# Kernel tuning notes

Hardware: AMD Instinct MI355X
Metric: run time of the kernel (lower is better)

## Reference

```python
import jax, jax.numpy as jnp
import numpy as np

N = 50000
E = 800000
IN_DIM = 128
HEADS = 4
OUT_DIM = 32
TOT = HEADS * OUT_DIM  # 128 == IN_DIM -> residual_proj is None
LN_EPS = 1e-5
NEG_SLOPE = 0.2


def setup_inputs() -> dict:
    key = jax.random.key(0)
    ks = jax.random.split(key, 10)
    x = jax.random.normal(ks[0], (N, IN_DIM), dtype=jnp.float32)
    # random edges guaranteed src != dst (PyG GATv2Conv removes then re-adds self loops)
    src = jax.random.randint(ks[1], (E,), 0, N)
    off = jax.random.randint(ks[2], (E,), 1, N)
    dst = (src + off) % N
    edge_index = jnp.stack([src, dst]).astype(jnp.int64)
    # glorot-style init for weights
    sc = 1.0 / np.sqrt(IN_DIM)
    W_l = jax.random.uniform(ks[3], (IN_DIM, TOT), jnp.float32, -sc, sc)
    b_l = jnp.zeros((TOT,), jnp.float32)
    W_r = jax.random.uniform(ks[4], (IN_DIM, TOT), jnp.float32, -sc, sc)
    b_r = jnp.zeros((TOT,), jnp.float32)
    att = jax.random.uniform(ks[5], (HEADS, OUT_DIM), jnp.float32, -sc, sc)
    bias = jnp.zeros((TOT,), jnp.float32)
    ln_g = jnp.ones((TOT,), jnp.float32)
    ln_b = jnp.zeros((TOT,), jnp.float32)
    return {"x": x, "edge_index": edge_index, "W_l": W_l, "b_l": b_l,
            "W_r": W_r, "b_r": b_r, "att": att, "bias": bias,
            "ln_g": ln_g, "ln_b": ln_b}


def _gatv2_layer(x, src, dst, W_l, b_l, W_r, b_r, att, bias, ln_g, ln_b):
    n = x.shape[0]
    # GATv2Conv: x_l = lin_l(x) (source/messages), x_r = lin_r(x) (target)
    xl = (x @ W_l + b_l).reshape(n, HEADS, OUT_DIM)
    xr = (x @ W_r + b_r).reshape(n, HEADS, OUT_DIM)
    m = xl[src] + xr[dst]                               # [E+N, H, D]
    s = jnp.einsum('ehd,hd->eh', jax.nn.leaky_relu(m, NEG_SLOPE), att)
    # per-destination softmax (every node has a self loop -> no empty segments)
    smax = jax.ops.segment_max(s, dst, num_segments=n)  # [N, H]
    e = jnp.exp(s - smax[dst])
    denom = jax.ops.segment_sum(e, dst, num_segments=n)
    alpha = e / denom[dst]                              # [E+N, H]
    out = jax.ops.segment_sum(alpha[..., None] * xl[src], dst, num_segments=n)
    out = out.reshape(n, TOT) + bias
    out = out + x                                       # residual (in_dim == total_out_dim)
    mu = jnp.mean(out, axis=-1, keepdims=True)
    var = jnp.mean(jnp.square(out - mu), axis=-1, keepdims=True)
    y = (out - mu) / jnp.sqrt(var + LN_EPS) * ln_g + ln_b
    return jax.nn.elu(y)


def reference(x, edge_index, W_l, b_l, W_r, b_r, att, bias, ln_g, ln_b):
    n = x.shape[0]
    loops = jnp.arange(n, dtype=edge_index.dtype)
    src = jnp.concatenate([edge_index[0], loops])
    dst = jnp.concatenate([edge_index[1], loops])
    return _gatv2_layer(x, src, dst, W_l, b_l, W_r, b_r, att, bias, ln_g, ln_b)
```

## Files before the change

### kernel.cpp

```cpp
#include <hip/hip_runtime.h>

#define N_NODES 50000
#define E_EDGES 800000
#define M_TOTAL (E_EDGES + N_NODES)
#define IN_DIM 128
#define HEADS 4
#define OUT_DIM 32
#define TOT 128
#define LN_EPS 1e-5f
#define NEG_SLOPE 0.2f
#define LOG2E 1.4426950408889634f

#define SCAN_NBLK ((N_NODES + 255) / 256)
#define GEMM_NBLK ((N_NODES + 63) / 64)
#define HIST_NBLK 64
#define EPB 13312
#define SEPB (EPB / 8)
#define SCAT_NBLK (HIST_NBLK * 8)

typedef __bf16 bf16x8 __attribute__((ext_vector_type(8)));
typedef float  f32x4  __attribute__((ext_vector_type(4)));
typedef _Float16 h2   __attribute__((ext_vector_type(2)));

__device__ __forceinline__ float quad_sum(float p) {
    p += __int_as_float(__builtin_amdgcn_update_dpp(
        0, __float_as_int(p), 0xB1 , 0xF, 0xF, true));
    p += __int_as_float(__builtin_amdgcn_update_dpp(
        0, __float_as_int(p), 0x4E , 0xF, 0xF, true));
    return p;
}

__global__ __launch_bounds__(256) void wthist_kernel(
    const int* __restrict__ dsts,
    const float* __restrict__ Wl, const float* __restrict__ Wr,
    unsigned* __restrict__ WT, unsigned char* __restrict__ HP,
    unsigned char* __restrict__ rank8) {
    __shared__ unsigned cnt[N_NODES / 8];
    const int b = blockIdx.x, t = threadIdx.x;
    if (b < 64) {
        const int u = b * 256 + t;
        const int col = u >> 6, k2 = u & 63;
        const float* __restrict__ W = (col < 128) ? Wl : Wr;
        const int c = col & 127;
        union { __bf16 bb[2]; unsigned uu; } p;
        p.bb[0] = (__bf16)W[(2 * k2) * TOT + c];
        p.bb[1] = (__bf16)W[(2 * k2 + 1) * TOT + c];
        WT[col * 64 + k2] = p.uu;
        return;
    }
    const int hb = b - 64;
    const int m_begin = hb * EPB;
    const int m_end = min(m_begin + EPB, M_TOTAL);
    for (int i = t; i < N_NODES / 8; i += 256) cnt[i] = 0;
    __syncthreads();
    for (int m0 = m_begin + t * 4; m0 < m_end; m0 += 1024) {
        int d[4];
        if (m0 < E_EDGES) {
            const int4 dv = *(const int4*)&dsts[m0];
            d[0] = dv.x; d[1] = dv.y; d[2] = dv.z; d[3] = dv.w;
        } else {
            d[0] = m0 - E_EDGES; d[1] = d[0] + 1; d[2] = d[0] + 2; d[3] = d[0] + 3;
        }
        uchar4 r;
        unsigned old, sh;
        sh = (d[0] & 7) * 4; old = atomicAdd(&cnt[d[0] >> 3], 1u << sh);
        r.x = (unsigned char)((old >> sh) & 15u);
        sh = (d[1] & 7) * 4; old = atomicAdd(&cnt[d[1] >> 3], 1u << sh);
        r.y = (unsigned char)((old >> sh) & 15u);
        sh = (d[2] & 7) * 4; old = atomicAdd(&cnt[d[2] >> 3], 1u << sh);
        r.z = (unsigned char)((old >> sh) & 15u);
        sh = (d[3] & 7) * 4; old = atomicAdd(&cnt[d[3] >> 3], 1u << sh);
        r.w = (unsigned char)((old >> sh) & 15u);
        *(uchar4*)&rank8[m0] = r;
    }
    __syncthreads();
    unsigned* __restrict__ Hrow = (unsigned*)(HP + (size_t)hb * N_NODES);
    for (int i = t; i < N_NODES / 8; i += 256) {
        const unsigned w = cnt[i];
        const unsigned lo = (w & 15u) | (((w >> 4) & 15u) << 8) |
                            (((w >> 8) & 15u) << 16) | (((w >> 12) & 15u) << 24);
        const unsigned hi = ((w >> 16) & 15u) | (((w >> 20) & 15u) << 8) |
                            (((w >> 24) & 15u) << 16) | (((w >> 28) & 15u) << 24);
        *(uint2*)&Hrow[2 * i] = make_uint2(lo, hi);
    }
}

__global__ __launch_bounds__(256) void scan1_kernel(
    unsigned char* __restrict__ HP,
    int* __restrict__ rowptr, int* __restrict__ blockSums) {
    __shared__ int sh[256];
    const int t = threadIdx.x;
    const int i = blockIdx.x * 256 + t;
    int tot = 0;
    if (i < N_NODES) {
        int run = 0;
#pragma unroll 16
        for (int b = 0; b < HIST_NBLK; ++b) {
            const int h = HP[(size_t)b * N_NODES + i];
            HP[(size_t)b * N_NODES + i] = (unsigned char)run;
            run += h;
        }
        tot = run;
    }
    sh[t] = tot;
    __syncthreads();
#pragma unroll
    for (int off = 1; off < 256; off <<= 1) {
        int u = (t >= off) ? sh[t - off] : 0;
        __syncthreads();
        sh[t] += u;
        __syncthreads();
    }
    if (i < N_NODES) rowptr[i] = sh[t] - tot;
    if (t == 255) blockSums[blockIdx.x] = sh[255];
}

__global__ __launch_bounds__(256) void scan23_kernel(
    const int* __restrict__ blockSums,
    int* __restrict__ rowptr ,
    unsigned short* __restrict__ sorted16) {
    __shared__ int sh[256];
    const int t = threadIdx.x;
    const int v0 = (t < SCAN_NBLK) ? blockSums[t] : 0;
    sh[t] = v0;
    __syncthreads();
#pragma unroll
    for (int off = 1; off < 256; off <<= 1) {
        int u = (t >= off) ? sh[t - off] : 0;
        __syncthreads();
        sh[t] += u;
        __syncthreads();
    }
    const int blockOff = (blockIdx.x == 0) ? 0 : sh[blockIdx.x - 1];
    const int i = blockIdx.x * 256 + t;
    if (i < N_NODES) rowptr[i] += blockOff;
    if (i == 0) rowptr[N_NODES] = M_TOTAL;
    if (blockIdx.x == 0 && t < 32) sorted16[M_TOTAL + t] = 0;
}

__global__ __launch_bounds__(256) void gemmscatter_kernel(
    const float* __restrict__ x, const unsigned* __restrict__ WT,
    const float* __restrict__ bl, const float* __restrict__ br,
    unsigned* __restrict__ xlb, unsigned* __restrict__ xrb,
    const int* __restrict__ srcs, const int* __restrict__ dsts,
    const int* __restrict__ rowptr, const unsigned char* __restrict__ P,
    const unsigned char* __restrict__ rank8,
    unsigned short* __restrict__ sorted16) {
    __shared__ float epi[4][16][66];
    __shared__ unsigned Bs[64][68];
    const int t = threadIdx.x;
    if (blockIdx.x >= GEMM_NBLK) {
        const int sb = blockIdx.x - GEMM_NBLK;
        const int hb = sb >> 3;
        const unsigned char* __restrict__ Pb = P + (size_t)hb * N_NODES;
        const int eb = hb * EPB + (sb & 7) * SEPB;
        const int ee = min(eb + SEPB, M_TOTAL);
        for (int m0 = eb + t * 4; m0 < ee; m0 += 1024) {
            int s[4], d[4];
            if (m0 < E_EDGES) {
                const int4 sv = *(const int4*)&srcs[m0];
                const int4 dv = *(const int4*)&dsts[m0];
                s[0] = sv.x; s[1] = sv.y; s[2] = sv.z; s[3] = sv.w;
                d[0] = dv.x; d[1] = dv.y; d[2] = dv.z; d[3] = dv.w;
            } else {
                s[0] = d[0] = m0 - E_EDGES;
                s[1] = d[1] = d[0] + 1; s[2] = d[2] = d[0] + 2; s[3] = d[3] = d[0] + 3;
            }
            const uchar4 r = *(const uchar4*)&rank8[m0];
            sorted16[rowptr[d[0]] + (int)Pb[d[0]] + (int)r.x] = (unsigned short)s[0];
            sorted16[rowptr[d[1]] + (int)Pb[d[1]] + (int)r.y] = (unsigned short)s[1];
            sorted16[rowptr[d[2]] + (int)Pb[d[2]] + (int)r.z] = (unsigned short)s[2];
            sorted16[rowptr[d[3]] + (int)Pb[d[3]] + (int)r.w] = (unsigned short)s[3];
        }
        return;
    }
    const int w = t >> 6, lane = t & 63;
    const int q = lane >> 4, ln = lane & 15;
    const int m0 = blockIdx.x * 64;

    const int row = min(m0 + w * 16 + ln, N_NODES - 1);
    const float* __restrict__ xrow = x + (size_t)row * IN_DIM;
    bf16x8 A[4];
#pragma unroll
    for (int c = 0; c < 4; ++c) {
        const float4 v0 = *(const float4*)&xrow[c * 32 + q * 8];
        const float4 v1 = *(const float4*)&xrow[c * 32 + q * 8 + 4];
        bf16x8 a;
        a[0] = (__bf16)v0.x; a[1] = (__bf16)v0.y; a[2] = (__bf16)v0.z; a[3] = (__bf16)v0.w;
        a[4] = (__bf16)v1.x; a[5] = (__bf16)v1.y; a[6] = (__bf16)v1.z; a[7] = (__bf16)v1.w;
        A[c] = a;
    }

    const int mr = lane >> 2, cg2 = (lane & 3) * 16;
    const int grow = m0 + w * 16 + mr;
#pragma unroll
    for (int g = 0; g < 4; ++g) {
        const int n0 = g * 64;
        __syncthreads();
        {
            const unsigned* __restrict__ src = WT + n0 * 64;
#pragma unroll
            for (int it = 0; it < 4; ++it) {
                const int dw = t * 4 + it * 1024;
                const uint4 v = *(const uint4*)&src[dw];
                *(uint4*)&Bs[dw >> 6][dw & 63] = v;
            }
        }
        __syncthreads();
        const float* __restrict__ bvec = (g < 2) ? bl : br;
        f32x4 acc[4];
#pragma unroll
        for (int nt = 0; nt < 4; ++nt) {
            const float b = bvec[(n0 & 127) + nt * 16 + ln];
            acc[nt] = (f32x4){b, b, b, b};
        }
#pragma unroll
        for (int nt = 0; nt < 4; ++nt) {
#pragma unroll
            for (int c = 0; c < 4; ++c) {
                const bf16x8 B = *(const bf16x8*)&Bs[nt * 16 + ln][c * 16 + q * 4];
                acc[nt] = __builtin_amdgcn_mfma_f32_16x16x32_bf16(A[c], B, acc[nt], 0, 0, 0);
            }
        }
#pragma unroll
        for (int nt = 0; nt < 4; ++nt)
#pragma unroll
            for (int r = 0; r < 4; ++r)
                epi[w][q * 4 + r][nt * 16 + ln] = acc[nt][r];

        if (grow < N_NODES) {
            unsigned p[8];
#pragma unroll
            for (int i = 0; i < 8; ++i) {
                union { _Float16 h[2]; unsigned u; } pk;
                pk.h[0] = (_Float16)epi[w][mr][cg2 + 2 * i];
                pk.h[1] = (_Float16)epi[w][mr][cg2 + 2 * i + 1];
                p[i] = pk.u;
            }
            unsigned* __restrict__ dst = ((g < 2) ? xlb : xrb) +
                (size_t)grow * 64 + (g & 1) * 32 + (cg2 >> 1);
            *(uint4*)&dst[0] = make_uint4(p[0], p[1], p[2], p[3]);
            *(uint4*)&dst[4] = make_uint4(p[4], p[5], p[6], p[7]);
        }
    }
}

__global__ __launch_bounds__(256) void gat_kernel(
    const int* __restrict__ rowptr, const unsigned short* __restrict__ sorted16,
    const unsigned* __restrict__ xlb, const unsigned* __restrict__ xrb,
    const float* __restrict__ att, const float* __restrict__ x,
    const float* __restrict__ bias, const float* __restrict__ g,
    const float* __restrict__ bvec, float* __restrict__ out) {
    const int d = blockIdx.x * 4 + (threadIdx.x >> 6);
    const int lane = threadIdx.x & 63;
    const int ln = lane & 15, q = lane >> 4;
    if (d >= N_NODES) return;

    h2 xrh[4], ath[4];
    {
        const uint4 ur = *(const uint4*)&xrb[(size_t)d * 64 + 4 * ln];
        union { uint4 u; h2 h[4]; } cr; cr.u = ur;
        xrh[0] = cr.h[0]; xrh[1] = cr.h[1]; xrh[2] = cr.h[2]; xrh[3] = cr.h[3];
        const float4 a0 = *(const float4*)&att[8 * ln];
        const float4 a1 = *(const float4*)&att[8 * ln + 4];
        ath[0][0] = (_Float16)(a0.x * LOG2E); ath[0][1] = (_Float16)(a0.y * LOG2E);
        ath[1][0] = (_Float16)(a0.z * LOG2E); ath[1][1] = (_Float16)(a0.w * LOG2E);
        ath[2][0] = (_Float16)(a1.x * LOG2E); ath[2][1] = (_Float16)(a1.y * LOG2E);
        ath[3][0] = (_Float16)(a1.z * LOG2E); ath[3][1] = (_Float16)(a1.w * LOG2E);
    }
    const h2 slope = (h2){(_Float16)NEG_SLOPE, (_Float16)NEG_SLOPE};
    const int beg = rowptr[d], end = rowptr[d + 1];

    float l = 0.f;
    h2 acc4[4];
#pragma unroll
    for (int k = 0; k < 4; ++k) acc4[k] = (h2){(_Float16)0.f, (_Float16)0.f};

    uint4 u0, u1;
    {
        const int sA0 = (int)sorted16[min(beg + q, end - 1)];
        const int sA1 = (int)sorted16[min(beg + 4 + q, end - 1)];
        u0 = *(const uint4*)&xlb[(size_t)sA0 * 64 + 4 * ln];
        u1 = *(const uint4*)&xlb[(size_t)sA1 * 64 + 4 * ln];
    }
    int sB0 = (int)sorted16[min(beg + 8 + q, end - 1)];
    int sB1 = (int)sorted16[min(beg + 12 + q, end - 1)];

    for (int base = beg; base < end; base += 8) {
        const int sC0 = (int)sorted16[min(base + 16 + q, end - 1)];
        const int sC1 = (int)sorted16[min(base + 20 + q, end - 1)];
        const uint4 un0 = *(const uint4*)&xlb[(size_t)sB0 * 64 + 4 * ln];
        const uint4 un1 = *(const uint4*)&xlb[(size_t)sB1 * 64 + 4 * ln];

        union { unsigned uu; h2 h; } a0, a1, a2, a3, b0, b1, b2, b3;
        a0.uu = u0.x; a1.uu = u0.y; a2.uu = u0.z; a3.uu = u0.w;
        b0.uu = u1.x; b1.uu = u1.y; b2.uu = u1.z; b3.uu = u1.w;
        h2 mA0 = a0.h + xrh[0], mA1 = a1.h + xrh[1];
        h2 mA2 = a2.h + xrh[2], mA3 = a3.h + xrh[3];
        h2 mB0 = b0.h + xrh[0], mB1 = b1.h + xrh[1];
        h2 mB2 = b2.h + xrh[2], mB3 = b3.h + xrh[3];
        mA0 = __builtin_elementwise_max(mA0, mA0 * slope);
        mA1 = __builtin_elementwise_max(mA1, mA1 * slope);
        mA2 = __builtin_elementwise_max(mA2, mA2 * slope);
        mA3 = __builtin_elementwise_max(mA3, mA3 * slope);
        mB0 = __builtin_elementwise_max(mB0, mB0 * slope);
        mB1 = __builtin_elementwise_max(mB1, mB1 * slope);
        mB2 = __builtin_elementwise_max(mB2, mB2 * slope);
        mB3 = __builtin_elementwise_max(mB3, mB3 * slope);
        float p0 = __builtin_amdgcn_fdot2(mA0, ath[0], 0.0f, false);
        p0 = __builtin_amdgcn_fdot2(mA1, ath[1], p0, false);
        p0 = __builtin_amdgcn_fdot2(mA2, ath[2], p0, false);
        p0 = __builtin_amdgcn_fdot2(mA3, ath[3], p0, false);
        float p1 = __builtin_amdgcn_fdot2(mB0, ath[0], 0.0f, false);
        p1 = __builtin_amdgcn_fdot2(mB1, ath[1], p1, false);
        p1 = __builtin_amdgcn_fdot2(mB2, ath[2], p1, false);
        p1 = __builtin_amdgcn_fdot2(mB3, ath[3], p1, false);
        p0 = quad_sum(p0);
        p1 = quad_sum(p1);
        const float e0 = (base + q < end) ? exp2f(p0) : 0.f;
        const float e1 = (base + 4 + q < end) ? exp2f(p1) : 0.f;
        l += e0 + e1;
        const _Float16 eh0 = (_Float16)e0, eh1 = (_Float16)e1;
        const h2 e20 = (h2){eh0, eh0}, e21 = (h2){eh1, eh1};
        acc4[0] += e20 * a0.h; acc4[0] += e21 * b0.h;
        acc4[1] += e20 * a1.h; acc4[1] += e21 * b1.h;
        acc4[2] += e20 * a2.h; acc4[2] += e21 * b2.h;
        acc4[3] += e20 * a3.h; acc4[3] += e21 * b3.h;

        u0 = un0; u1 = un1; sB0 = sC0; sB1 = sC1;
    }

#pragma unroll
    for (int off = 16; off <= 32; off <<= 1) {
        l += __shfl_xor(l, off, 64);
#pragma unroll
        for (int k = 0; k < 4; ++k) {
            union { h2 h; int i; } tmp; tmp.h = acc4[k];
            tmp.i = __shfl_xor(tmp.i, off, 64);
            acc4[k] += tmp.h;
        }
    }
    float acc[8];
#pragma unroll
    for (int k = 0; k < 4; ++k) {
        acc[2 * k]     = (float)acc4[k][0];
        acc[2 * k + 1] = (float)acc4[k][1];
    }

    const float inv_l = 1.0f / l;
    const float4 xv0 = *(const float4*)&x[(size_t)d * TOT + 8 * ln];
    const float4 xv1 = *(const float4*)&x[(size_t)d * TOT + 8 * ln + 4];
    const float4 bi0 = *(const float4*)&bias[8 * ln];
    const float4 bi1 = *(const float4*)&bias[8 * ln + 4];
    float v[8];
    v[0] = fmaf(acc[0], inv_l, bi0.x + xv0.x);
    v[1] = fmaf(acc[1], inv_l, bi0.y + xv0.y);
    v[2] = fmaf(acc[2], inv_l, bi0.z + xv0.z);
    v[3] = fmaf(acc[3], inv_l, bi0.w + xv0.w);
    v[4] = fmaf(acc[4], inv_l, bi1.x + xv1.x);
    v[5] = fmaf(acc[5], inv_l, bi1.y + xv1.y);
    v[6] = fmaf(acc[6], inv_l, bi1.z + xv1.z);
    v[7] = fmaf(acc[7], inv_l, bi1.w + xv1.w);
    float sum = 0.f, sq = 0.f;
#pragma unroll
    for (int k = 0; k < 8; ++k) { sum += v[k]; sq = fmaf(v[k], v[k], sq); }
#pragma unroll
    for (int off = 1; off <= 8; off <<= 1) {
        sum += __shfl_xor(sum, off, 64);
        sq  += __shfl_xor(sq,  off, 64);
    }
    const float mu  = sum * (1.0f / TOT);
    const float var = sq * (1.0f / TOT) - mu * mu;
    const float inv = rsqrtf(var + LN_EPS);
    const float4 g0 = *(const float4*)&g[8 * ln];
    const float4 g1 = *(const float4*)&g[8 * ln + 4];
    const float4 b0 = *(const float4*)&bvec[8 * ln];
    const float4 b1 = *(const float4*)&bvec[8 * ln + 4];
    float y[8];
    y[0] = (v[0] - mu) * inv * g0.x + b0.x;
    y[1] = (v[1] - mu) * inv * g0.y + b0.y;
    y[2] = (v[2] - mu) * inv * g0.z + b0.z;
    y[3] = (v[3] - mu) * inv * g0.w + b0.w;
    y[4] = (v[4] - mu) * inv * g1.x + b1.x;
    y[5] = (v[5] - mu) * inv * g1.y + b1.y;
    y[6] = (v[6] - mu) * inv * g1.z + b1.z;
    y[7] = (v[7] - mu) * inv * g1.w + b1.w;
#pragma unroll
    for (int k = 0; k < 8; ++k) y[k] = y[k] > 0.f ? y[k] : __expf(y[k]) - 1.f;
    if (q < 2) {
        float4 o = (q == 0) ? make_float4(y[0], y[1], y[2], y[3])
                            : make_float4(y[4], y[5], y[6], y[7]);
        *(float4*)&out[(size_t)d * TOT + 8 * ln + 4 * q] = o;
    }
}

extern "C" void kernel_launch(void* const* d_in, const int* in_sizes, int n_in,
                              void* d_out, int out_size, void* d_ws, size_t ws_size,
                              hipStream_t stream) {
    const float* x    = (const float*)d_in[0];
    const int*   ei   = (const int*)d_in[1];
    const float* Wl   = (const float*)d_in[2];
    const float* bl   = (const float*)d_in[3];
    const float* Wr   = (const float*)d_in[4];
    const float* br   = (const float*)d_in[5];
    const float* att  = (const float*)d_in[6];
    const float* bias = (const float*)d_in[7];
    const float* ln_g = (const float*)d_in[8];
    const float* ln_b = (const float*)d_in[9];
    const int* srcs = ei;
    const int* dsts = ei + E_EDGES;

    unsigned* xlb = (unsigned*)d_ws;
    unsigned* xrb = xlb + (size_t)N_NODES * 64;
    int*   rowptr     = (int*)(xrb + (size_t)N_NODES * 64);
    int*   blockSums  = rowptr + N_NODES + 1;
    unsigned* WT      = (unsigned*)(blockSums + SCAN_NBLK + 4);
    unsigned char* HP = (unsigned char*)(WT + 256 * 64);
    unsigned short* sorted16 = (unsigned short*)(HP + (size_t)HIST_NBLK * N_NODES);
    unsigned char*  rank8    = (unsigned char*)(sorted16 + M_TOTAL + 32);

    wthist_kernel<<<64 + HIST_NBLK, 256, 0, stream>>>(dsts, Wl, Wr, WT, HP, rank8);
    scan1_kernel<<<SCAN_NBLK, 256, 0, stream>>>(HP, rowptr, blockSums);
    scan23_kernel<<<SCAN_NBLK, 256, 0, stream>>>(blockSums, rowptr, sorted16);
    gemmscatter_kernel<<<GEMM_NBLK + SCAT_NBLK, 256, 0, stream>>>(
        x, WT, bl, br, xlb, xrb, srcs, dsts, rowptr, HP, rank8, sorted16);
    gat_kernel<<<(N_NODES + 3) / 4, 256, 0, stream>>>(rowptr, sorted16, xlb, xrb, att, x,
                                                      bias, ln_g, ln_b, (float*)d_out);
}
```

Baseline: 172.0 us.

## Fuse two-pass scan into single-pass lookback scan and deepen gather prefetch

```diff
diff --git a/kernel.cpp b/kernel.cpp
--- a/kernel.cpp
+++ b/kernel.cpp
@@ -34,10 +34,11 @@
     const int* __restrict__ dsts,
     const float* __restrict__ Wl, const float* __restrict__ Wr,
     unsigned* __restrict__ WT, unsigned char* __restrict__ HP,
-    unsigned char* __restrict__ rank8) {
+    unsigned char* __restrict__ rank8, unsigned* __restrict__ pub) {
     __shared__ unsigned cnt[N_NODES / 8];
     const int b = blockIdx.x, t = threadIdx.x;
     if (b < 64) {
+        if (b == 0 && t < SCAN_NBLK) pub[t] = 0;
         const int u = b * 256 + t;
         const int col = u >> 6, k2 = u & 63;
         const float* __restrict__ W = (col < 128) ? Wl : Wr;
@@ -85,12 +86,12 @@
     }
 }
 
-__global__ __launch_bounds__(256) void scan1_kernel(
-    unsigned char* __restrict__ HP,
-    int* __restrict__ rowptr, int* __restrict__ blockSums) {
+__global__ __launch_bounds__(256) void scan_kernel(
+    unsigned char* __restrict__ HP, int* __restrict__ rowptr,
+    unsigned* __restrict__ pub, unsigned short* __restrict__ sorted16) {
     __shared__ int sh[256];
-    const int t = threadIdx.x;
-    const int i = blockIdx.x * 256 + t;
+    const int t = threadIdx.x, bid = blockIdx.x;
+    const int i = bid * 256 + t;
     int tot = 0;
     if (i < N_NODES) {
         int run = 0;
@@ -111,31 +112,26 @@
         sh[t] += u;
         __syncthreads();
     }
-    if (i < N_NODES) rowptr[i] = sh[t] - tot;
-    if (t == 255) blockSums[blockIdx.x] = sh[255];
-}
-
-__global__ __launch_bounds__(256) void scan23_kernel(
-    const int* __restrict__ blockSums,
-    int* __restrict__ rowptr ,
-    unsigned short* __restrict__ sorted16) {
-    __shared__ int sh[256];
-    const int t = threadIdx.x;
-    const int v0 = (t < SCAN_NBLK) ? blockSums[t] : 0;
-    sh[t] = v0;
+    const int excl = sh[t] - tot;
+    if (t == 255) atomicExch(&pub[bid], (unsigned)(sh[255] + 1));
+    int part = 0;
+    for (int j = t; j < bid; j += 256) {
+        unsigned v;
+        do { v = atomicAdd(&pub[j], 0u); } while (v == 0u);
+        part += (int)v - 1;
+    }
     __syncthreads();
-#pragma unroll
-    for (int off = 1; off < 256; off <<= 1) {
-        int u = (t >= off) ? sh[t - off] : 0;
+    sh[t] = part;
+    __syncthreads();
+#pragma unroll
+    for (int off = 128; off >= 1; off >>= 1) {
+        if (t < off) sh[t] += sh[t + off];
         __syncthreads();
-        sh[t] += u;
-        __syncthreads();
-    }
-    const int blockOff = (blockIdx.x == 0) ? 0 : sh[blockIdx.x - 1];
-    const int i = blockIdx.x * 256 + t;
-    if (i < N_NODES) rowptr[i] += blockOff;
+    }
+    const int blockOff = sh[0];
+    if (i < N_NODES) rowptr[i] = excl + blockOff;
     if (i == 0) rowptr[N_NODES] = M_TOTAL;
-    if (blockIdx.x == 0 && t < 32) sorted16[M_TOTAL + t] = 0;
+    if (bid == 0 && t < 32) sorted16[M_TOTAL + t] = 0;
 }
 
 __global__ __launch_bounds__(256) void gemmscatter_kernel(
@@ -276,21 +272,25 @@
 #pragma unroll
     for (int k = 0; k < 4; ++k) acc4[k] = (h2){(_Float16)0.f, (_Float16)0.f};
 
-    uint4 u0, u1;
+    uint4 u0, u1, v0, v1;
     {
         const int sA0 = (int)sorted16[min(beg + q, end - 1)];
         const int sA1 = (int)sorted16[min(beg + 4 + q, end - 1)];
         u0 = *(const uint4*)&xlb[(size_t)sA0 * 64 + 4 * ln];
         u1 = *(const uint4*)&xlb[(size_t)sA1 * 64 + 4 * ln];
-    }
-    int sB0 = (int)sorted16[min(beg + 8 + q, end - 1)];
-    int sB1 = (int)sorted16[min(beg + 12 + q, end - 1)];
+        const int sB0 = (int)sorted16[min(beg + 8 + q, end - 1)];
+        const int sB1 = (int)sorted16[min(beg + 12 + q, end - 1)];
+        v0 = *(const uint4*)&xlb[(size_t)sB0 * 64 + 4 * ln];
+        v1 = *(const uint4*)&xlb[(size_t)sB1 * 64 + 4 * ln];
+    }
+    int sC0 = (int)sorted16[min(beg + 16 + q, end - 1)];
+    int sC1 = (int)sorted16[min(beg + 20 + q, end - 1)];
 
     for (int base = beg; base < end; base += 8) {
-        const int sC0 = (int)sorted16[min(base + 16 + q, end - 1)];
-        const int sC1 = (int)sorted16[min(base + 20 + q, end - 1)];
-        const uint4 un0 = *(const uint4*)&xlb[(size_t)sB0 * 64 + 4 * ln];
-        const uint4 un1 = *(const uint4*)&xlb[(size_t)sB1 * 64 + 4 * ln];
+        const int sD0 = (int)sorted16[min(base + 24 + q, end - 1)];
+        const int sD1 = (int)sorted16[min(base + 28 + q, end - 1)];
+        const uint4 w0 = *(const uint4*)&xlb[(size_t)sC0 * 64 + 4 * ln];
+        const uint4 w1 = *(const uint4*)&xlb[(size_t)sC1 * 64 + 4 * ln];
 
         union { unsigned uu; h2 h; } a0, a1, a2, a3, b0, b1, b2, b3;
         a0.uu = u0.x; a1.uu = u0.y; a2.uu = u0.z; a3.uu = u0.w;
@@ -327,7 +327,7 @@
         acc4[2] += e20 * a2.h; acc4[2] += e21 * b2.h;
         acc4[3] += e20 * a3.h; acc4[3] += e21 * b3.h;
 
-        u0 = un0; u1 = un1; sB0 = sC0; sB1 = sC1;
+        u0 = v0; u1 = v1; v0 = w0; v1 = w1; sC0 = sD0; sC1 = sD1;
     }
 
 #pragma unroll
@@ -413,15 +413,14 @@
     unsigned* xlb = (unsigned*)d_ws;
     unsigned* xrb = xlb + (size_t)N_NODES * 64;
     int*   rowptr     = (int*)(xrb + (size_t)N_NODES * 64);
-    int*   blockSums  = rowptr + N_NODES + 1;
-    unsigned* WT      = (unsigned*)(blockSums + SCAN_NBLK + 4);
+    unsigned* pub     = (unsigned*)(rowptr + N_NODES + 1);
+    unsigned* WT      = (unsigned*)(pub + SCAN_NBLK + 3);
     unsigned char* HP = (unsigned char*)(WT + 256 * 64);
     unsigned short* sorted16 = (unsigned short*)(HP + (size_t)HIST_NBLK * N_NODES);
     unsigned char*  rank8    = (unsigned char*)(sorted16 + M_TOTAL + 32);
 
-    wthist_kernel<<<64 + HIST_NBLK, 256, 0, stream>>>(dsts, Wl, Wr, WT, HP, rank8);
-    scan1_kernel<<<SCAN_NBLK, 256, 0, stream>>>(HP, rowptr, blockSums);
-    scan23_kernel<<<SCAN_NBLK, 256, 0, stream>>>(blockSums, rowptr, sorted16);
+    wthist_kernel<<<64 + HIST_NBLK, 256, 0, stream>>>(dsts, Wl, Wr, WT, HP, rank8, pub);
+    scan_kernel<<<SCAN_NBLK, 256, 0, stream>>>(HP, rowptr, pub, sorted16);
     gemmscatter_kernel<<<GEMM_NBLK + SCAT_NBLK, 256, 0, stream>>>(
         x, WT, bl, br, xlb, xrb, srcs, dsts, rowptr, HP, rank8, sorted16);
     gat_kernel<<<(N_NODES + 3) / 4, 256, 0, stream>>>(rowptr, sorted16, xlb, xrb, att, x,
```

Result: no change. 172.8 us (+0.4%).
